# Performance work log

Measured on AMD Instinct MI355X. Metric: run time of the kernel, lower is better.

## Reference

```python
import jax, jax.numpy as jnp
import numpy as np

H = 8      # num_heads
DH = 80    # head_dim = embed_dim // num_heads


def setup_inputs() -> dict:
    key = jax.random.key(0)
    ks = jax.random.split(key, 7)
    B, T, S = 8, 4096, 77
    hidden, embed, ctx = 640, 640, 768
    sc_h = 1.0 / np.sqrt(hidden)
    sc_c = 1.0 / np.sqrt(ctx)
    sc_e = 1.0 / np.sqrt(embed)
    return {
        "tokens": jax.random.normal(ks[0], (B, T, hidden), jnp.float32),
        "context": jax.random.normal(ks[1], (B, S, ctx), jnp.float32),
        "Wq": jax.random.normal(ks[2], (hidden, embed), jnp.float32) * sc_h,
        "Wk": jax.random.normal(ks[3], (ctx, embed), jnp.float32) * sc_c,
        "Wv": jax.random.normal(ks[4], (ctx, embed), jnp.float32) * sc_c,
        "Wo": jax.random.normal(ks[5], (embed, hidden), jnp.float32) * sc_e,
        "bo": jnp.zeros((hidden,), jnp.float32),
    }


def reference(tokens, context, Wq, Wk, Wv, Wo, bo):
    B, T, _ = tokens.shape
    S = context.shape[1]
    Q = (tokens @ Wq).reshape(B, T, H, DH)    # B T H D
    K = (context @ Wk).reshape(B, S, H, DH)   # B S H D
    V = (context @ Wv).reshape(B, S, H, DH)
    scores = jnp.einsum('bthd,bshd->bhts', Q, K) / jnp.sqrt(jnp.float32(DH))
    attn = jax.nn.softmax(scores, axis=-1)    # B H T S
    ctx_vecs = jnp.einsum('bhts,bshd->bthd', attn, V).reshape(B, T, H * DH)
    return ctx_vecs @ Wo + bo
```

## Files before the change

### kernel.cpp

```cpp
#include <hip/hip_runtime.h>
#include <hip/hip_bf16.h>
#include <hip/hip_fp16.h>

typedef __attribute__((ext_vector_type(4))) float f32x4;
typedef __attribute__((ext_vector_type(8))) _Float16 f16x8;
typedef __attribute__((ext_vector_type(8))) unsigned short u16x8;

__device__ __forceinline__ unsigned short f2h(float f) {
    _Float16 h = (_Float16)f;
    return __builtin_bit_cast(unsigned short, h);
}

#define GLOAD_LDS16(gp, lp) __builtin_amdgcn_global_load_lds( \
    (const __attribute__((address_space(1))) void*)(gp), \
    (__attribute__((address_space(3))) void*)(lp), 16, 0, 0)
#define PRIO1() __builtin_amdgcn_s_setprio(1)
#define PRIO0() __builtin_amdgcn_s_setprio(0)
#define WAITVM(LIT) do { asm volatile("s_waitcnt vmcnt(" #LIT ")" ::: "memory"); \
                         __builtin_amdgcn_sched_barrier(0); } while (0)
#define BARND() do { asm volatile("s_waitcnt lgkmcnt(0)" ::: "memory"); \
                     __builtin_amdgcn_sched_barrier(0); \
                     __builtin_amdgcn_s_barrier(); \
                     __builtin_amdgcn_sched_barrier(0); } while (0)

__global__ void cvt_kernel(const float* __restrict__ in, ushort* __restrict__ out, int n4) {
    int stride = gridDim.x * blockDim.x;
    for (int i = blockIdx.x * blockDim.x + threadIdx.x; i < n4; i += stride) {
        float4 v = ((const float4*)in)[i];
        ushort4 o;
        o.x = f2h(v.x); o.y = f2h(v.y); o.z = f2h(v.z); o.w = f2h(v.w);
        ((ushort4*)out)[i] = o;
    }
}

__global__ void transpose_cvt2(const float* __restrict__ Wk, const float* __restrict__ Wv,
                               ushort* __restrict__ WkvT) {
    __shared__ float tile[32][33];
    const int z = blockIdx.z;
    const float* src = z ? Wv : Wk;
    ushort* dst = WkvT + (size_t)z * 640 * 768;
    const int R = 768, C = 640;
    int tx = threadIdx.x, ty = threadIdx.y;
    int c = blockIdx.x * 32 + tx;
    int r0 = blockIdx.y * 32;
#pragma unroll
    for (int i = ty; i < 32; i += 8) {
        int r = r0 + i;
        tile[i][tx] = (r < R && c < C) ? src[(size_t)r * C + c] : 0.f;
    }
    __syncthreads();
    int rr = r0 + tx;
    int c0 = blockIdx.x * 32;
#pragma unroll
    for (int i = ty; i < 32; i += 8) {
        int cc = c0 + i;
        if (cc < C && rr < R) dst[(size_t)cc * R + rr] = f2h(tile[tx][i]);
    }
}

__global__ void pack_wfrag2(const float* __restrict__ Wq, const float* __restrict__ Wo,
                            ushort* __restrict__ WqF, ushort* __restrict__ WoF) {
    int g = blockIdx.x * 256 + threadIdx.x;
    if (g >= 51200) return;
    const float* W = blockIdx.y ? Wo : Wq;
    ushort* WF = blockIdx.y ? WoF : WqF;
    int lane = g & 63;
    int fi = (g >> 6) % 10;
    int kt = ((g >> 6) / 10) % 10;
    int h  = (g >> 6) / 100;
    int ni = fi >> 1, kk = fi & 1;
    int n  = h * 80 + ni * 16 + (lane & 15);
    int k0 = kt * 64 + kk * 32 + (lane >> 4) * 8;
    u16x8 o;
#pragma unroll
    for (int e = 0; e < 8; ++e) o[e] = f2h(W[(size_t)(k0 + e) * 640 + n]);
    *(u16x8*)&WF[(size_t)g * 8] = o;
}

__global__ void pack_kvfrag(const ushort* __restrict__ KVb,
                            ushort* __restrict__ KF, ushort* __restrict__ VF) {
    int g = blockIdx.x * 256 + threadIdx.x;
    if (g >= 61440) return;
    int lane = g & 63;
    int fi = (g >> 6) % 15;
    int bh = (g >> 6) / 15;
    int b = bh >> 3, h = bh & 7;
    int ni = fi / 3, kk = fi % 3;
    int l15 = lane & 15, lhi = lane >> 4;
    int sr = ni * 16 + l15; if (sr > 76) sr = 76;
    int d0 = kk * 32 + lhi * 8;
    u16x8 ko, vo;
#pragma unroll
    for (int e = 0; e < 8; ++e)
        ko[e] = KVb[((size_t)b * 77 + sr) * 1280 + h * 80 + d0 + e];
    int dv = ni * 16 + l15;
    int s0 = kk * 32 + lhi * 8;
#pragma unroll
    for (int e = 0; e < 8; ++e) {
        int s = s0 + e;
        vo[e] = (s < 77) ? KVb[((size_t)b * 77 + s) * 1280 + 640 + h * 80 + dv] : (ushort)0;
    }
    *(u16x8*)&KF[(size_t)g * 8] = ko;
    *(u16x8*)&VF[(size_t)g * 8] = vo;
}

template<int OUT_F16, int HAS_BIAS>
__global__ __launch_bounds__(256) void gemm_bt(
    const ushort* __restrict__ A, const ushort* __restrict__ Bt,
    void* __restrict__ C, const float* __restrict__ bias,
    int M, int N, int K)
{
    __shared__ ushort As[128 * 64];
    __shared__ ushort Bs[128 * 64];
    const int tid = threadIdx.x;
    const int lane = tid & 63;
    const int w = tid >> 6;
    const int wr = (w >> 1) * 64, wc = (w & 1) * 64;
    const int m0 = blockIdx.x * 128, n0 = blockIdx.y * 128;
    const int l15 = lane & 15, lhi = lane >> 4;

    f32x4 acc[4][4] = {};

    for (int k0 = 0; k0 < K; k0 += 64) {
        __syncthreads();
#pragma unroll
        for (int i = 0; i < 4; ++i) {
            int c = i * 256 + tid;
            int m = m0 + (c >> 3);
            if (m > M - 1) m = M - 1;
            GLOAD_LDS16(A + (size_t)m * K + k0 + (c & 7) * 8, &As[c * 8]);
        }
#pragma unroll
        for (int i = 0; i < 4; ++i) {
            int c = i * 256 + tid;
            GLOAD_LDS16(Bt + (size_t)(n0 + (c >> 3)) * K + k0 + (c & 7) * 8, &Bs[c * 8]);
        }
        __syncthreads();
#pragma unroll
        for (int kk = 0; kk < 2; ++kk) {
            f16x8 af[4], bfr[4];
#pragma unroll
            for (int mi = 0; mi < 4; ++mi)
                af[mi] = *(const f16x8*)&As[(wr + mi * 16 + l15) * 64 + kk * 32 + lhi * 8];
#pragma unroll
            for (int ni = 0; ni < 4; ++ni)
                bfr[ni] = *(const f16x8*)&Bs[(wc + ni * 16 + l15) * 64 + kk * 32 + lhi * 8];
#pragma unroll
            for (int mi = 0; mi < 4; ++mi)
#pragma unroll
                for (int ni = 0; ni < 4; ++ni)
                    acc[mi][ni] = __builtin_amdgcn_mfma_f32_16x16x32_f16(
                        af[mi], bfr[ni], acc[mi][ni], 0, 0, 0);
        }
    }

#pragma unroll
    for (int mi = 0; mi < 4; ++mi)
#pragma unroll
        for (int ni = 0; ni < 4; ++ni)
#pragma unroll
            for (int r = 0; r < 4; ++r) {
                int row = m0 + wr + mi * 16 + lhi * 4 + r;
                int col = n0 + wc + ni * 16 + l15;
                if (row < M) {
                    float v = acc[mi][ni][r];
                    if (HAS_BIAS) v += bias[col];
                    if (OUT_F16) ((ushort*)C)[(size_t)row * N + col] = f2h(v);
                    else         ((float*)C)[(size_t)row * N + col] = v;
                }
            }
}

__global__ __launch_bounds__(512, 2) void fused_attn(
    const float* __restrict__ tokens, const ushort* __restrict__ WqF,
    const ushort* __restrict__ KF, const ushort* __restrict__ VF,
    const ushort* __restrict__ WoF, const float* __restrict__ bo,
    float* __restrict__ out)
{
    __shared__ __align__(16) ushort lds[81920];
    const int tid = threadIdx.x;
    const int lane = tid & 63;
    const int w = tid >> 6;
    const int l15 = lane & 15, lhi = lane >> 4;
    const int tt = blockIdx.x, b = blockIdx.y;
    const size_t rowbase = (size_t)b * 4096 + (size_t)tt * 64;

    const ushort* WqFb = WqF + (size_t)w * 10 * 5120;
    const ushort* WoFb = WoF + (size_t)w * 10 * 5120;
    const ushort* KFb  = KF + (size_t)(b * 8 + w) * 15 * 512;
    const ushort* VFb  = VF + (size_t)(b * 8 + w) * 15 * 512;
    const int qstrip = 8192 + w * 7680;
    const int ostrip = 40960 + w * 5120;

    const int srow = tid >> 3;
    const int sc8  = tid & 7;
    const int sphys = (sc8 ^ (srow & 7)) * 8;

#define STAGE_LOAD(C, A0, B0) do { \
    const float* p_ = tokens + (rowbase + srow) * 640 + (C) * 64 + sc8 * 8; \
    A0 = ((const float4*)p_)[0]; B0 = ((const float4*)p_)[1]; \
} while (0)
#define STAGE_WRITE(BUF, A0, B0) do { \
    u16x8 o_; \
    o_[0]=f2h(A0.x); o_[1]=f2h(A0.y); o_[2]=f2h(A0.z); o_[3]=f2h(A0.w); \
    o_[4]=f2h(B0.x); o_[5]=f2h(B0.y); o_[6]=f2h(B0.z); o_[7]=f2h(B0.w); \
    *(u16x8*)&lds[(BUF) * 4096 + srow * 64 + sphys] = o_; \
} while (0)

#define GLOADB_Q(HX) do { \
    if ((HX) <= 19) { \
        const ushort* s_ = WqFb + ((HX) >> 1) * 5120 + ((HX) & 1) * 512 + lane * 8; \
        _Pragma("unroll") for (int f_ = 0; f_ < 5; ++f_) \
            GLOAD_LDS16(s_ + f_ * 1024, &lds[qstrip + ((HX) % 3) * 2560 + f_ * 512]); \
    } \
} while (0)
#define GLOADB_O(HX) do { \
    if ((HX) <= 19) { \
        const ushort* s_ = WoFb + ((HX) >> 1) * 5120 + ((HX) & 1) * 512 + lane * 8; \
        _Pragma("unroll") for (int f_ = 0; f_ < 5; ++f_) \
            GLOAD_LDS16(s_ + f_ * 1024, &lds[ostrip + ((HX) & 1) * 2560 + f_ * 512]); \
    } \
} while (0)

    f32x4 acc[4][5];
#define ZACC() do { \
    _Pragma("unroll") for (int i_ = 0; i_ < 4; ++i_) \
    _Pragma("unroll") for (int j_ = 0; j_ < 5; ++j_) \
        acc[i_][j_] = (f32x4){0.f, 0.f, 0.f, 0.f}; \
} while (0)

#define MFMA_Q(KT, KK) do { \
    f16x8 bf_[5]; \
    _Pragma("unroll") for (int ni = 0; ni < 5; ++ni) \
        bf_[ni] = *(const f16x8*)&lds[qstrip + ((2*(KT)+(KK)) % 3) * 2560 + ni * 512 + lane * 8]; \
    PRIO1(); \
    _Pragma("unroll") for (int mi = 0; mi < 4; ++mi) { \
        int row_ = mi * 16 + l15; \
        f16x8 a_ = *(const f16x8*)&lds[((KT) & 1) * 4096 + row_ * 64 + (((KK)*4 + lhi) ^ (row_ & 7)) * 8]; \
        _Pragma("unroll") for (int ni = 0; ni < 5; ++ni) \
            acc[mi][ni] = __builtin_amdgcn_mfma_f32_16x16x32_f16(a_, bf_[ni], acc[mi][ni], 0, 0, 0); \
    } \
    PRIO0(); \
} while (0)
#define MFMA_O(HX) do { \
    f16x8 bf_[5]; \
    _Pragma("unroll") for (int ni = 0; ni < 5; ++ni) \
        bf_[ni] = *(const f16x8*)&lds[ostrip + ((HX) & 1) * 2560 + ni * 512 + lane * 8]; \
    PRIO1(); \
    _Pragma("unroll") for (int mi = 0; mi < 4; ++mi) { \
        int row_ = mi * 16 + l15; \
        f16x8 a_ = *(const f16x8*)&lds[row_ * 640 + (((HX) >> 1) * 8 + ((((HX) & 1)*4 + lhi) ^ (row_ & 7))) * 8]; \
        _Pragma("unroll") for (int ni = 0; ni < 5; ++ni) \
            acc[mi][ni] = __builtin_amdgcn_mfma_f32_16x16x32_f16(a_, bf_[ni], acc[mi][ni], 0, 0, 0); \
    } \
    PRIO0(); \
} while (0)

#define QKT(KT, WA, WB, LA, LB, WRA, WRB) do { \
    if ((KT) < 8) STAGE_LOAD((KT) + 2, LA, LB); \
    GLOADB_Q(2*(KT) + 2); \
    WAITVM(WA); \
    if ((KT) < 9) STAGE_WRITE(((KT)+1) & 1, WRA, WRB); \
    MFMA_Q(KT, 0); \
    GLOADB_Q(2*(KT) + 3); \
    WAITVM(WB); \
    MFMA_Q(KT, 1); \
    BARND(); \
} while (0)

    float4 sA0, sB0, sA1, sB1;
    STAGE_LOAD(0, sA0, sB0);
    STAGE_LOAD(1, sA1, sB1);
    GLOADB_Q(0);
    GLOADB_Q(1);
    WAITVM(10);
    STAGE_WRITE(0, sA0, sB0);
    BARND();

    ZACC();
    QKT(0, 10, 10, sA0, sB0, sA1, sB1);
    QKT(1, 10, 10, sA1, sB1, sA0, sB0);
    QKT(2, 10, 10, sA0, sB0, sA1, sB1);
    QKT(3, 10, 10, sA1, sB1, sA0, sB0);
    QKT(4, 10, 10, sA0, sB0, sA1, sB1);
    QKT(5, 10, 10, sA1, sB1, sA0, sB0);
    QKT(6, 10, 10, sA0, sB0, sA1, sB1);
    QKT(7, 10, 10, sA1, sB1, sA0, sB0);
    QKT(8, 10, 10, sA0, sB0, sA1, sB1);
    QKT(9,  5,  0, sA0, sB0, sA1, sB1);
#undef QKT

    const int qoff = w * 5120;
#pragma unroll
    for (int mi = 0; mi < 4; ++mi)
#pragma unroll
        for (int ni = 0; ni < 5; ++ni)
#pragma unroll
            for (int r = 0; r < 4; ++r)
                lds[qoff + (mi*16 + lhi*4 + r)*80 + ni*16 + l15] = f2h(acc[mi][ni][r]);
    __builtin_amdgcn_sched_barrier(0);

    const f16x8 zf = {};
    f16x8 PE[5], PO[5];
#define ATT_KK(PC, PN, FB, KK, NKK, DOPF) do { \
    if (DOPF) { \
        _Pragma("unroll") for (int f = 0; f < 5; ++f) \
            (PN)[f] = *(const f16x8*)((FB) + (f * 3 + (NKK)) * 512 + lane * 8); \
    } \
    const int kcol = ((KK) < 2) ? ((KK)*32 + lhi*8) : (64 + (lhi & 1)*8); \
    PRIO1(); \
    _Pragma("unroll") for (int mi = 0; mi < 4; ++mi) { \
        f16x8 aq_ = *(const f16x8*)&lds[qoff + (mi*16 + l15)*80 + kcol]; \
        if ((KK) == 2 && lhi >= 2) aq_ = zf; \
        _Pragma("unroll") for (int ni = 0; ni < 5; ++ni) \
            acc[mi][ni] = __builtin_amdgcn_mfma_f32_16x16x32_f16(aq_, (PC)[ni], acc[mi][ni], 0, 0, 0); \
    } \
    PRIO0(); \
} while (0)

    ZACC();
#pragma unroll
    for (int f = 0; f < 5; ++f)
        PE[f] = *(const f16x8*)(KFb + (f * 3) * 512 + lane * 8);
    ATT_KK(PE, PO, KFb, 0, 1, 1);
    ATT_KK(PO, PE, KFb, 1, 2, 1);
    ATT_KK(PE, PO, KFb, 2, 0, 0);
    __builtin_amdgcn_sched_barrier(0);

    const float sc = 0.11180339887498949f;
#pragma unroll
    for (int mi = 0; mi < 4; ++mi)
#pragma unroll
        for (int r = 0; r < 4; ++r) {
            float v0 = acc[mi][0][r]*sc, v1 = acc[mi][1][r]*sc, v2 = acc[mi][2][r]*sc,
                  v3 = acc[mi][3][r]*sc, v4 = acc[mi][4][r]*sc;
            bool ok4 = l15 < 13;
            float mx = fmaxf(fmaxf(v0, v1), fmaxf(v2, v3));
            if (ok4) mx = fmaxf(mx, v4);
#pragma unroll
            for (int off = 1; off < 16; off <<= 1) mx = fmaxf(mx, __shfl_xor(mx, off, 16));
            float p0 = __expf(v0-mx), p1 = __expf(v1-mx), p2 = __expf(v2-mx), p3 = __expf(v3-mx);
            float p4 = ok4 ? __expf(v4-mx) : 0.f;
            float sm = p0+p1+p2+p3+p4;
#pragma unroll
            for (int off = 1; off < 16; off <<= 1) sm += __shfl_xor(sm, off, 16);
            float inv = 1.f / sm;
            int row = mi*16 + lhi*4 + r;
            lds[qoff + row*80 + 0*16 + l15] = f2h(p0*inv);
            lds[qoff + row*80 + 1*16 + l15] = f2h(p1*inv);
            lds[qoff + row*80 + 2*16 + l15] = f2h(p2*inv);
            lds[qoff + row*80 + 3*16 + l15] = f2h(p3*inv);
            lds[qoff + row*80 + 4*16 + l15] = f2h(p4*inv);
        }
    __builtin_amdgcn_sched_barrier(0);

    ZACC();
#pragma unroll
    for (int f = 0; f < 5; ++f)
        PE[f] = *(const f16x8*)(VFb + (f * 3) * 512 + lane * 8);
    ATT_KK(PE, PO, VFb, 0, 1, 1);
    ATT_KK(PO, PE, VFb, 1, 2, 1);
    ATT_KK(PE, PO, VFb, 2, 0, 0);
#undef ATT_KK

    GLOADB_O(0);
    BARND();

#pragma unroll
    for (int mi = 0; mi < 4; ++mi)
#pragma unroll
        for (int ni = 0; ni < 5; ++ni)
#pragma unroll
            for (int r = 0; r < 4; ++r) {
                int row = mi*16 + lhi*4 + r;
                int col = w*80 + ni*16 + l15;
                int slot = col >> 3;
                int phys = (slot & ~7) | ((slot ^ row) & 7);
                lds[row*640 + phys*8 + (col & 7)] = f2h(acc[mi][ni][r]);
            }
    BARND();

    ZACC();
#define OH(HX, W) do { GLOADB_O((HX) + 1); WAITVM(W); MFMA_O(HX); } while (0)
    OH(0, 5);  OH(1, 5);  OH(2, 5);  OH(3, 5);  OH(4, 5);
    OH(5, 5);  OH(6, 5);  OH(7, 5);  OH(8, 5);  OH(9, 5);
    OH(10, 5); OH(11, 5); OH(12, 5); OH(13, 5); OH(14, 5);
    OH(15, 5); OH(16, 5); OH(17, 5); OH(18, 5); OH(19, 0);
#undef OH

#pragma unroll
    for (int ni = 0; ni < 5; ++ni) {
        int col = w*80 + ni*16 + l15;
        float bvl = bo[col];
#pragma unroll
        for (int mi = 0; mi < 4; ++mi)
#pragma unroll
            for (int r = 0; r < 4; ++r)
                out[(rowbase + mi*16 + lhi*4 + r) * 640 + col] = acc[mi][ni][r] + bvl;
    }
#undef STAGE_LOAD
#undef STAGE_WRITE
#undef GLOADB_Q
#undef GLOADB_O
#undef MFMA_Q
#undef MFMA_O
#undef ZACC
}

extern "C" void kernel_launch(void* const* d_in, const int* in_sizes, int n_in,
                              void* d_out, int out_size, void* d_ws, size_t ws_size,
                              hipStream_t stream) {
    (void)in_sizes; (void)n_in; (void)out_size; (void)ws_size;
    const float* tokens  = (const float*)d_in[0];
    const float* context = (const float*)d_in[1];
    const float* Wq = (const float*)d_in[2];
    const float* Wk = (const float*)d_in[3];
    const float* Wv = (const float*)d_in[4];
    const float* Wo = (const float*)d_in[5];
    const float* bo = (const float*)d_in[6];
    float* out = (float*)d_out;

    ushort* ws   = (ushort*)d_ws;
    ushort* ctx16 = ws;
    ushort* WkvT = ctx16 + (size_t)616 * 768;
    ushort* KVb  = WkvT + (size_t)1280 * 768;
    ushort* WqF  = KVb  + (size_t)616 * 1280;
    ushort* WoF  = WqF  + (size_t)640 * 640;
    ushort* KF   = WoF  + (size_t)640 * 640;
    ushort* VF   = KF   + (size_t)61440 * 8;

    cvt_kernel<<<462, 256, 0, stream>>>(context, ctx16, 616 * 768 / 4);
    transpose_cvt2<<<dim3(20, 24, 2), dim3(32, 8), 0, stream>>>(Wk, Wv, WkvT);
    pack_wfrag2<<<dim3(200, 2), 256, 0, stream>>>(Wq, Wo, WqF, WoF);
    gemm_bt<1, 0><<<dim3(5, 10), 256, 0, stream>>>(ctx16, WkvT, KVb, nullptr, 616, 1280, 768);
    pack_kvfrag<<<240, 256, 0, stream>>>(KVb, KF, VF);
    fused_attn<<<dim3(64, 8), 512, 0, stream>>>(tokens, WqF, KF, VF, WoF, bo, out);
}
```

Baseline: 124.6 us.

## Fold Wq·K^T and V·Wo per batch to skip in-kernel attention GEMMs

```diff
diff --git a/kernel.cpp b/kernel.cpp
--- a/kernel.cpp
+++ b/kernel.cpp
@@ -33,13 +33,17 @@
     }
 }
 
-__global__ void transpose_cvt2(const float* __restrict__ Wk, const float* __restrict__ Wv,
-                               ushort* __restrict__ WkvT) {
+__global__ void transpose_cvt3(const float* __restrict__ Wk, const float* __restrict__ Wv,
+                               const float* __restrict__ Wo,
+                               ushort* __restrict__ WkvT, ushort* __restrict__ WoT) {
     __shared__ float tile[32][33];
     const int z = blockIdx.z;
-    const float* src = z ? Wv : Wk;
-    ushort* dst = WkvT + (size_t)z * 640 * 768;
-    const int R = 768, C = 640;
+    const float* src; ushort* dst; int R;
+    const int C = 640;
+    if (z == 0)      { src = Wk; dst = WkvT; R = 768; }
+    else if (z == 1) { src = Wv; dst = WkvT + (size_t)640 * 768; R = 768; }
+    else             { src = Wo; dst = WoT; R = 640; }
+    if (blockIdx.y * 32 >= (unsigned)R) return;
     int tx = threadIdx.x, ty = threadIdx.y;
     int c = blockIdx.x * 32 + tx;
     int r0 = blockIdx.y * 32;
@@ -56,52 +60,6 @@
         int cc = c0 + i;
         if (cc < C && rr < R) dst[(size_t)cc * R + rr] = f2h(tile[tx][i]);
     }
-}
-
-__global__ void pack_wfrag2(const float* __restrict__ Wq, const float* __restrict__ Wo,
-                            ushort* __restrict__ WqF, ushort* __restrict__ WoF) {
-    int g = blockIdx.x * 256 + threadIdx.x;
-    if (g >= 51200) return;
-    const float* W = blockIdx.y ? Wo : Wq;
-    ushort* WF = blockIdx.y ? WoF : WqF;
-    int lane = g & 63;
-    int fi = (g >> 6) % 10;
-    int kt = ((g >> 6) / 10) % 10;
-    int h  = (g >> 6) / 100;
-    int ni = fi >> 1, kk = fi & 1;
-    int n  = h * 80 + ni * 16 + (lane & 15);
-    int k0 = kt * 64 + kk * 32 + (lane >> 4) * 8;
-    u16x8 o;
-#pragma unroll
-    for (int e = 0; e < 8; ++e) o[e] = f2h(W[(size_t)(k0 + e) * 640 + n]);
-    *(u16x8*)&WF[(size_t)g * 8] = o;
-}
-
-__global__ void pack_kvfrag(const ushort* __restrict__ KVb,
-                            ushort* __restrict__ KF, ushort* __restrict__ VF) {
-    int g = blockIdx.x * 256 + threadIdx.x;
-    if (g >= 61440) return;
-    int lane = g & 63;
-    int fi = (g >> 6) % 15;
-    int bh = (g >> 6) / 15;
-    int b = bh >> 3, h = bh & 7;
-    int ni = fi / 3, kk = fi % 3;
-    int l15 = lane & 15, lhi = lane >> 4;
-    int sr = ni * 16 + l15; if (sr > 76) sr = 76;
-    int d0 = kk * 32 + lhi * 8;
-    u16x8 ko, vo;
-#pragma unroll
-    for (int e = 0; e < 8; ++e)
-        ko[e] = KVb[((size_t)b * 77 + sr) * 1280 + h * 80 + d0 + e];
-    int dv = ni * 16 + l15;
-    int s0 = kk * 32 + lhi * 8;
-#pragma unroll
-    for (int e = 0; e < 8; ++e) {
-        int s = s0 + e;
-        vo[e] = (s < 77) ? KVb[((size_t)b * 77 + s) * 1280 + 640 + h * 80 + dv] : (ushort)0;
-    }
-    *(u16x8*)&KF[(size_t)g * 8] = ko;
-    *(u16x8*)&VF[(size_t)g * 8] = vo;
 }
 
 template<int OUT_F16, int HAS_BIAS>
@@ -171,10 +129,139 @@
             }
 }
 
+__global__ __launch_bounds__(512) void fold_wk(
+    const float* __restrict__ Wq, const ushort* __restrict__ KVb, ushort* __restrict__ WKp)
+{
+    __shared__ ushort Al[640 * 88];
+    __shared__ ushort Bl[80 * 88];
+    const int tid = threadIdx.x, lane = tid & 63, w = tid >> 6;
+    const int l15 = lane & 15, lhi = lane >> 4;
+    const int h = blockIdx.x, b = blockIdx.y;
+    for (int i = tid; i < 6400; i += 512) {
+        int c = i / 10, oc = i % 10;
+        const float* p = Wq + (size_t)c * 640 + h * 80 + oc * 8;
+        u16x8 o;
+#pragma unroll
+        for (int e = 0; e < 8; ++e) o[e] = f2h(p[e]);
+        *(u16x8*)&Al[c * 88 + oc * 8] = o;
+    }
+    for (int i = tid; i < 800; i += 512) {
+        int s = i / 10, oc = i % 10;
+        u16x8 o = {};
+        if (s < 77) {
+            const ushort* p = KVb + ((size_t)b * 77 + s) * 1280 + h * 80 + oc * 8;
+#pragma unroll
+            for (int e = 0; e < 8; ++e) o[e] = p[e];
+        }
+        *(u16x8*)&Bl[s * 88 + oc * 8] = o;
+    }
+    __syncthreads();
+    const int wb = w * 80;
+    f32x4 acc[5][5] = {};
+    const f16x8 zf = {};
+#pragma unroll
+    for (int kk = 0; kk < 3; ++kk) {
+        const int kcol = (kk < 2) ? (kk * 32 + lhi * 8) : (64 + (lhi & 1) * 8);
+        f16x8 bf[5];
+#pragma unroll
+        for (int ni = 0; ni < 5; ++ni)
+            bf[ni] = *(const f16x8*)&Bl[(ni * 16 + l15) * 88 + kcol];
+#pragma unroll
+        for (int mi = 0; mi < 5; ++mi) {
+            f16x8 af = *(const f16x8*)&Al[(wb + mi * 16 + l15) * 88 + kcol];
+            if (kk == 2 && lhi >= 2) af = zf;
+#pragma unroll
+            for (int ni = 0; ni < 5; ++ni)
+                acc[mi][ni] = __builtin_amdgcn_mfma_f32_16x16x32_f16(af, bf[ni], acc[mi][ni], 0, 0, 0);
+        }
+    }
+    ushort* dst = WKp + (size_t)b * 409600 + h * 80;
+#pragma unroll
+    for (int mi = 0; mi < 5; ++mi)
+#pragma unroll
+        for (int ni = 0; ni < 5; ++ni)
+#pragma unroll
+            for (int r = 0; r < 4; ++r) {
+                int c = wb + mi * 16 + lhi * 4 + r;
+                int s = ni * 16 + l15;
+                dst[(size_t)c * 640 + s] = f2h(acc[mi][ni][r]);
+            }
+}
+
+__global__ __launch_bounds__(512) void fold_vw(
+    const ushort* __restrict__ KVb, const ushort* __restrict__ WoT, ushort* __restrict__ VWp)
+{
+    __shared__ ushort Al[80 * 88];
+    const int tid = threadIdx.x, lane = tid & 63, w = tid >> 6;
+    const int l15 = lane & 15, lhi = lane >> 4;
+    const int h = blockIdx.x, b = blockIdx.y;
+    for (int i = tid; i < 800; i += 512) {
+        int s = i / 10, oc = i % 10;
+        u16x8 o = {};
+        if (s < 77) {
+            const ushort* p = KVb + ((size_t)b * 77 + s) * 1280 + 640 + h * 80 + oc * 8;
+#pragma unroll
+            for (int e = 0; e < 8; ++e) o[e] = p[e];
+        }
+        *(u16x8*)&Al[s * 88 + oc * 8] = o;
+    }
+    __syncthreads();
+    const int nb = w * 80;
+    f32x4 acc[5][5] = {};
+    const f16x8 zf = {};
+#pragma unroll
+    for (int kk = 0; kk < 3; ++kk) {
+        const int kcol = (kk < 2) ? (kk * 32 + lhi * 8) : (64 + (lhi & 1) * 8);
+        f16x8 af[5];
+#pragma unroll
+        for (int mi = 0; mi < 5; ++mi) {
+            af[mi] = *(const f16x8*)&Al[(mi * 16 + l15) * 88 + kcol];
+            if (kk == 2 && lhi >= 2) af[mi] = zf;
+        }
+#pragma unroll
+        for (int ni = 0; ni < 5; ++ni) {
+            f16x8 bf = *(const f16x8*)(WoT + (size_t)(nb + ni * 16 + l15) * 640 + h * 80 + kcol);
+#pragma unroll
+            for (int mi = 0; mi < 5; ++mi)
+                acc[mi][ni] = __builtin_amdgcn_mfma_f32_16x16x32_f16(af[mi], bf, acc[mi][ni], 0, 0, 0);
+        }
+    }
+    ushort* dst = VWp + (size_t)b * 409600 + (size_t)(h * 80) * 640;
+#pragma unroll
+    for (int mi = 0; mi < 5; ++mi)
+#pragma unroll
+        for (int ni = 0; ni < 5; ++ni)
+#pragma unroll
+            for (int r = 0; r < 4; ++r) {
+                int s = mi * 16 + lhi * 4 + r;
+                int n = nb + ni * 16 + l15;
+                dst[(size_t)s * 640 + n] = f2h(acc[mi][ni][r]);
+            }
+}
+
+__global__ void pack_f(const ushort* __restrict__ WKp, const ushort* __restrict__ VWp,
+                       ushort* __restrict__ WKF, ushort* __restrict__ VWF) {
+    int g = blockIdx.x * 256 + threadIdx.x;
+    if (g >= 51200) return;
+    int b = blockIdx.y;
+    const ushort* src = (blockIdx.z ? VWp : WKp) + (size_t)b * 409600;
+    ushort* dst = (blockIdx.z ? VWF : WKF) + (size_t)b * 409600;
+    int lane = g & 63;
+    int fi = (g >> 6) % 10;
+    int kt = ((g >> 6) / 10) % 10;
+    int sl = (g >> 6) / 100;
+    int ni = fi >> 1, kk = fi & 1;
+    int n = sl * 80 + ni * 16 + (lane & 15);
+    int k0 = kt * 64 + kk * 32 + (lane >> 4) * 8;
+    u16x8 o;
+#pragma unroll
+    for (int e = 0; e < 8; ++e) o[e] = src[(size_t)(k0 + e) * 640 + n];
+    *(u16x8*)&dst[(size_t)g * 8] = o;
+}
+
 __global__ __launch_bounds__(512, 2) void fused_attn(
-    const float* __restrict__ tokens, const ushort* __restrict__ WqF,
-    const ushort* __restrict__ KF, const ushort* __restrict__ VF,
-    const ushort* __restrict__ WoF, const float* __restrict__ bo,
+    const float* __restrict__ tokens, const ushort* __restrict__ WKF,
+    const ushort* __restrict__ VWF, const float* __restrict__ bo,
     float* __restrict__ out)
 {
     __shared__ __align__(16) ushort lds[81920];
@@ -182,13 +269,13 @@
     const int lane = tid & 63;
     const int w = tid >> 6;
     const int l15 = lane & 15, lhi = lane >> 4;
-    const int tt = blockIdx.x, b = blockIdx.y;
+    const int bid = blockIdx.x;
+    const int b = bid & 7;
+    const int tt = bid >> 3;
     const size_t rowbase = (size_t)b * 4096 + (size_t)tt * 64;
 
-    const ushort* WqFb = WqF + (size_t)w * 10 * 5120;
-    const ushort* WoFb = WoF + (size_t)w * 10 * 5120;
-    const ushort* KFb  = KF + (size_t)(b * 8 + w) * 15 * 512;
-    const ushort* VFb  = VF + (size_t)(b * 8 + w) * 15 * 512;
+    const ushort* WKFb = WKF + ((size_t)b * 800 + (size_t)w * 100) * 512;
+    const ushort* VWFb = VWF + ((size_t)b * 800 + (size_t)w * 100) * 512;
     const int qstrip = 8192 + w * 7680;
     const int ostrip = 40960 + w * 5120;
 
@@ -209,14 +296,14 @@
 
 #define GLOADB_Q(HX) do { \
     if ((HX) <= 19) { \
-        const ushort* s_ = WqFb + ((HX) >> 1) * 5120 + ((HX) & 1) * 512 + lane * 8; \
+        const ushort* s_ = WKFb + ((HX) >> 1) * 5120 + ((HX) & 1) * 512 + lane * 8; \
         _Pragma("unroll") for (int f_ = 0; f_ < 5; ++f_) \
             GLOAD_LDS16(s_ + f_ * 1024, &lds[qstrip + ((HX) % 3) * 2560 + f_ * 512]); \
     } \
 } while (0)
 #define GLOADB_O(HX) do { \
     if ((HX) <= 19) { \
-        const ushort* s_ = WoFb + ((HX) >> 1) * 5120 + ((HX) & 1) * 512 + lane * 8; \
+        const ushort* s_ = VWFb + ((HX) >> 1) * 5120 + ((HX) & 1) * 512 + lane * 8; \
         _Pragma("unroll") for (int f_ = 0; f_ < 5; ++f_) \
             GLOAD_LDS16(s_ + f_ * 1024, &lds[ostrip + ((HX) & 1) * 2560 + f_ * 512]); \
     } \
@@ -290,43 +377,6 @@
     QKT(9,  5,  0, sA0, sB0, sA1, sB1);
 #undef QKT
 
-    const int qoff = w * 5120;
-#pragma unroll
-    for (int mi = 0; mi < 4; ++mi)
-#pragma unroll
-        for (int ni = 0; ni < 5; ++ni)
-#pragma unroll
-            for (int r = 0; r < 4; ++r)
-                lds[qoff + (mi*16 + lhi*4 + r)*80 + ni*16 + l15] = f2h(acc[mi][ni][r]);
-    __builtin_amdgcn_sched_barrier(0);
-
-    const f16x8 zf = {};
-    f16x8 PE[5], PO[5];
-#define ATT_KK(PC, PN, FB, KK, NKK, DOPF) do { \
-    if (DOPF) { \
-        _Pragma("unroll") for (int f = 0; f < 5; ++f) \
-            (PN)[f] = *(const f16x8*)((FB) + (f * 3 + (NKK)) * 512 + lane * 8); \
-    } \
-    const int kcol = ((KK) < 2) ? ((KK)*32 + lhi*8) : (64 + (lhi & 1)*8); \
-    PRIO1(); \
-    _Pragma("unroll") for (int mi = 0; mi < 4; ++mi) { \
-        f16x8 aq_ = *(const f16x8*)&lds[qoff + (mi*16 + l15)*80 + kcol]; \
-        if ((KK) == 2 && lhi >= 2) aq_ = zf; \
-        _Pragma("unroll") for (int ni = 0; ni < 5; ++ni) \
-            acc[mi][ni] = __builtin_amdgcn_mfma_f32_16x16x32_f16(aq_, (PC)[ni], acc[mi][ni], 0, 0, 0); \
-    } \
-    PRIO0(); \
-} while (0)
-
-    ZACC();
-#pragma unroll
-    for (int f = 0; f < 5; ++f)
-        PE[f] = *(const f16x8*)(KFb + (f * 3) * 512 + lane * 8);
-    ATT_KK(PE, PO, KFb, 0, 1, 1);
-    ATT_KK(PO, PE, KFb, 1, 2, 1);
-    ATT_KK(PE, PO, KFb, 2, 0, 0);
-    __builtin_amdgcn_sched_barrier(0);
-
     const float sc = 0.11180339887498949f;
 #pragma unroll
     for (int mi = 0; mi < 4; ++mi)
@@ -346,41 +396,20 @@
             for (int off = 1; off < 16; off <<= 1) sm += __shfl_xor(sm, off, 16);
             float inv = 1.f / sm;
             int row = mi*16 + lhi*4 + r;
-            lds[qoff + row*80 + 0*16 + l15] = f2h(p0*inv);
-            lds[qoff + row*80 + 1*16 + l15] = f2h(p1*inv);
-            lds[qoff + row*80 + 2*16 + l15] = f2h(p2*inv);
-            lds[qoff + row*80 + 3*16 + l15] = f2h(p3*inv);
-            lds[qoff + row*80 + 4*16 + l15] = f2h(p4*inv);
-        }
-    __builtin_amdgcn_sched_barrier(0);
-
-    ZACC();
-#pragma unroll
-    for (int f = 0; f < 5; ++f)
-        PE[f] = *(const f16x8*)(VFb + (f * 3) * 512 + lane * 8);
-    ATT_KK(PE, PO, VFb, 0, 1, 1);
-    ATT_KK(PO, PE, VFb, 1, 2, 1);
-    ATT_KK(PE, PO, VFb, 2, 0, 0);
-#undef ATT_KK
-
-    GLOADB_O(0);
-    BARND();
-
-#pragma unroll
-    for (int mi = 0; mi < 4; ++mi)
-#pragma unroll
-        for (int ni = 0; ni < 5; ++ni)
-#pragma unroll
-            for (int r = 0; r < 4; ++r) {
-                int row = mi*16 + lhi*4 + r;
+            float pv0 = p0*inv, pv1 = p1*inv, pv2 = p2*inv, pv3 = p3*inv, pv4 = p4*inv;
+            float pvs[5] = {pv0, pv1, pv2, pv3, pv4};
+#pragma unroll
+            for (int ni = 0; ni < 5; ++ni) {
                 int col = w*80 + ni*16 + l15;
                 int slot = col >> 3;
                 int phys = (slot & ~7) | ((slot ^ row) & 7);
-                lds[row*640 + phys*8 + (col & 7)] = f2h(acc[mi][ni][r]);
+                lds[row*640 + phys*8 + (col & 7)] = f2h(pvs[ni]);
             }
+        }
     BARND();
 
     ZACC();
+    GLOADB_O(0);
 #define OH(HX, W) do { GLOADB_O((HX) + 1); WAITVM(W); MFMA_O(HX); } while (0)
     OH(0, 5);  OH(1, 5);  OH(2, 5);  OH(3, 5);  OH(4, 5);
     OH(5, 5);  OH(6, 5);  OH(7, 5);  OH(8, 5);  OH(9, 5);
@@ -423,16 +452,18 @@
     ushort* ws   = (ushort*)d_ws;
     ushort* ctx16 = ws;
     ushort* WkvT = ctx16 + (size_t)616 * 768;
-    ushort* KVb  = WkvT + (size_t)1280 * 768;
-    ushort* WqF  = KVb  + (size_t)616 * 1280;
-    ushort* WoF  = WqF  + (size_t)640 * 640;
-    ushort* KF   = WoF  + (size_t)640 * 640;
-    ushort* VF   = KF   + (size_t)61440 * 8;
+    ushort* WoT  = WkvT + (size_t)1280 * 768;
+    ushort* KVb  = WoT  + (size_t)640 * 640;
+    ushort* WKp  = KVb  + (size_t)616 * 1280;
+    ushort* VWp  = WKp  + (size_t)8 * 409600;
+    ushort* WKF  = VWp  + (size_t)8 * 409600;
+    ushort* VWF  = WKF  + (size_t)8 * 409600;
 
     cvt_kernel<<<462, 256, 0, stream>>>(context, ctx16, 616 * 768 / 4);
-    transpose_cvt2<<<dim3(20, 24, 2), dim3(32, 8), 0, stream>>>(Wk, Wv, WkvT);
-    pack_wfrag2<<<dim3(200, 2), 256, 0, stream>>>(Wq, Wo, WqF, WoF);
+    transpose_cvt3<<<dim3(20, 24, 3), dim3(32, 8), 0, stream>>>(Wk, Wv, Wo, WkvT, WoT);
     gemm_bt<1, 0><<<dim3(5, 10), 256, 0, stream>>>(ctx16, WkvT, KVb, nullptr, 616, 1280, 768);
-    pack_kvfrag<<<240, 256, 0, stream>>>(KVb, KF, VF);
-    fused_attn<<<dim3(64, 8), 512, 0, stream>>>(tokens, WqF, KF, VF, WoF, bo, out);
-}
+    fold_wk<<<dim3(8, 8), 512, 0, stream>>>(Wq, KVb, WKp);
+    fold_vw<<<dim3(8, 8), 512, 0, stream>>>(KVb, WoT, VWp);
+    pack_f<<<dim3(200, 8, 2), 256, 0, stream>>>(WKp, VWp, WKF, VWF);
+    fused_attn<<<512, 512, 0, stream>>>(tokens, WKF, VWF, bo, out);
+}
```

After: 140.4 us. 1.13x slower.
